# Optimization experiments

Hardware: AMD Instinct MI355X
Metric: run time of the kernel (lower is better)

The kernel has to match this reference:

```python
import jax, jax.numpy as jnp
import numpy as np

N_HEADS = 8
D_EMBED = 64
B, S = 2, 2048
ROPE_BASE = 10000.0


def apply_rope(x):
    # x: [b, h, s, d]; interleaved-pair rotary embedding over the s axis
    d = x.shape[-1]
    s = x.shape[-2]
    inv_freq = 1.0 / (ROPE_BASE ** (jnp.arange(0, d, 2, dtype=jnp.float32) / d))  # [d/2]
    angles = jnp.arange(s, dtype=jnp.float32)[:, None] * inv_freq[None, :]  # [s, d/2]
    cos = jnp.cos(angles)[None, None, :, :]
    sin = jnp.sin(angles)[None, None, :, :]
    x1 = x[..., 0::2]
    x2 = x[..., 1::2]
    out = jnp.stack([x1 * cos - x2 * sin, x1 * sin + x2 * cos], axis=-1)
    return out.reshape(x.shape)


def setup_inputs() -> dict:
    key = jax.random.key(0)
    ks = jax.random.split(key, 7)
    scale = 1.0 / np.sqrt(D_EMBED)
    return {
        "q": jax.random.normal(ks[0], (B, S, D_EMBED), dtype=jnp.float32),
        "k": jax.random.normal(ks[1], (B, S, D_EMBED), dtype=jnp.float32),
        "v": jax.random.normal(ks[2], (B, S, D_EMBED), dtype=jnp.float32),
        "W_q": jax.random.normal(ks[3], (N_HEADS, D_EMBED, D_EMBED), dtype=jnp.float32) * scale,
        "W_k": jax.random.normal(ks[4], (N_HEADS, D_EMBED, D_EMBED), dtype=jnp.float32) * scale,
        "W_v": jax.random.normal(ks[5], (N_HEADS, D_EMBED, D_EMBED), dtype=jnp.float32) * scale,
        "W_o": jax.random.normal(ks[6], (N_HEADS * D_EMBED, D_EMBED), dtype=jnp.float32) * scale,
    }


def reference(q, k, v, W_q, W_k, W_v, W_o):
    Bn, Sn, E = q.shape
    H = W_q.shape[0]
    qh = jnp.einsum('bsz,hzd->bhsd', q, W_q)
    kh = jnp.einsum('bsz,hzd->bhsd', k, W_k)
    vh = jnp.einsum('bsz,hzd->bhsd', v, W_v)
    qh = apply_rope(qh)
    kh = apply_rope(kh)
    attn_scaling = 1.0 / E  # note: 1/d, not 1/sqrt(d), per original
    scores = jnp.einsum('bhqd,bhkd->bhqk', qh, kh)
    causal = jnp.triu(jnp.ones((Sn, Sn), dtype=bool), k=1)
    scores = jnp.where(causal[None, None], -jnp.inf, scores) * attn_scaling
    probs = jax.nn.softmax(scores, axis=-1)
    # post-softmax diagonal zeroing (breaks normalization; this is the ICL twist)
    diag_mask = 1.0 - jnp.eye(Sn, dtype=probs.dtype)
    probs = probs * diag_mask[None, None]
    # NOTE: einsum 'bhzs,bhzd->bhsd' in the original contracts over the QUERY axis
    # (probs transposed): out[k-pos] = sum_q P[q, k-pos] * v[q]
    out = jnp.einsum('bhqk,bhqd->bhkd', probs, vh)
    out = out.transpose(0, 2, 1, 3).reshape(Bn, Sn, H * E)
    return jnp.einsum('bsz,zd->bsd', out, W_o)
```

## Files before the change

kernel.cpp:

```cpp
#include <hip/hip_runtime.h>
#include <hip/hip_bf16.h>
#include <math.h>

#define NH 8
#define D 64
#define BB 2
#define SS 2048
#define NBH (BB*NH)
#define LOG2E 1.4426950408889634f
#define KPAR 8
#define QPAR 4

typedef short bf16x8 __attribute__((ext_vector_type(8)));
typedef float f32x4 __attribute__((ext_vector_type(4)));

#define MFMA16(a,b,c) __builtin_amdgcn_mfma_f32_16x16x32_bf16((a),(b),(c),0,0,0)

__device__ inline int xcd_swz(int orig, int nwg) {
    int cpx = nwg >> 3;
    return (orig & 7) * cpx + (orig >> 3);
}

__device__ inline short f2bf(float f) {
    unsigned u = __float_as_uint(f);
    unsigned r = (u + 0x7fffu + ((u >> 16) & 1u)) >> 16;
    return (short)r;
}
__device__ inline float bf2f(short s) {
    return __uint_as_float(((unsigned)(unsigned short)s) << 16);
}
__device__ inline unsigned pack2bf(float a, float b) {
    __hip_bfloat162 hv = __float22bfloat162_rn(make_float2(a, b));
    unsigned u;
    __builtin_memcpy(&u, &hv, 4);
    return u;
}

__global__ __launch_bounds__(256) void wtrans_kernel(
    const float* __restrict__ Wq, const float* __restrict__ Wk,
    const float* __restrict__ Wv, const float* __restrict__ Wo,
    short* __restrict__ WqT, short* __restrict__ WkT, short* __restrict__ WvT,
    short* __restrict__ WoT) {
    int blk = blockIdx.x;
    int t = threadIdx.x;
    if (blk < 24) {
        int tensor = blk >> 3, h = blk & 7;
        const float* W = tensor == 0 ? Wq : (tensor == 1 ? Wk : Wv);
        short* WT = tensor == 0 ? WqT : (tensor == 1 ? WkT : WvT);
        __shared__ float wl[64][65];
        {
            int z = t >> 2, c0 = (t & 3) * 16;
            const float* src = W + (size_t)h * 4096 + (size_t)z * 64 + c0;
#pragma unroll
            for (int i = 0; i < 16; ++i) wl[z][c0 + i] = src[i];
        }
        __syncthreads();
        {
            int d = t >> 2, z0 = (t & 3) * 16;
            short* dst = WT + ((size_t)h * 64 + d) * 64 + z0;
#pragma unroll
            for (int i = 0; i < 16; ++i) dst[i] = f2bf(wl[z0 + i][d]);
        }
    } else {
        int idx = (blk - 24) * 256 + t;
        int d = idx >> 6;
        int zc = (idx & 63) * 32;
#pragma unroll
        for (int j = 0; j < 32; ++j) {
            int z = zc + j;
            WoT[(size_t)d * 2048 + z] = f2bf(Wo[(size_t)(z & 511) * 64 + d]);
        }
    }
}

__global__ __launch_bounds__(256) void proj_mfma_kernel(
    const float* __restrict__ xq, const float* __restrict__ xk,
    const float* __restrict__ xv,
    const short* __restrict__ WqT, const short* __restrict__ WkT,
    const short* __restrict__ WvT,
    short* __restrict__ qh, short* __restrict__ kh, short* __restrict__ vhT) {
    int blk = xcd_swz(blockIdx.x, 3 * NBH * 32);
    int tensor = blk / (NBH * 32);
    int rem = blk - tensor * (NBH * 32);
    int st = rem & 31, bh = rem >> 5;
    int h = bh & 7, b = bh >> 3;
    const float* x = tensor == 0 ? xq : (tensor == 1 ? xk : xv);
    const short* WT = tensor == 0 ? WqT : (tensor == 1 ? WkT : WvT);

    int t = threadIdx.x, w = t >> 6, lane = t & 63;
    int l15 = lane & 15, lg = lane >> 4;

    __shared__ short vt[64 * 64];

    int sA = st * 64 + w * 16 + l15;
    const float* xr = x + ((size_t)b * SS + sA) * D + lg * 8;
    bf16x8 a0, a1;
#pragma unroll
    for (int j = 0; j < 8; ++j) a0[j] = f2bf(xr[j]);
#pragma unroll
    for (int j = 0; j < 8; ++j) a1[j] = f2bf(xr[32 + j]);

    bf16x8 bfr[4][2];
#pragma unroll
    for (int ds_ = 0; ds_ < 4; ++ds_) {
        int d = ds_ * 16 + l15;
        const short* wp = WT + ((size_t)h * 64 + d) * 64 + lg * 8;
        bfr[ds_][0] = *(const bf16x8*)(wp);
        bfr[ds_][1] = *(const bf16x8*)(wp + 32);
    }

    f32x4 c[4];
#pragma unroll
    for (int ds_ = 0; ds_ < 4; ++ds_) {
        f32x4 z = {0.f, 0.f, 0.f, 0.f};
        z = MFMA16(a0, bfr[ds_][0], z);
        z = MFMA16(a1, bfr[ds_][1], z);
        c[ds_] = z;
    }

    int sbase = st * 64 + w * 16 + lg * 4;
    if (tensor < 2) {
        short* dst = tensor == 0 ? qh : kh;
        float scale = tensor == 0 ? (LOG2E / 64.0f) : 1.0f;
#pragma unroll
        for (int ds_ = 0; ds_ < 4; ++ds_) {
            int d = ds_ * 16 + l15;
            float invf = exp2f(-(float)(d & ~1) * (13.287712379549449f / 64.0f));
#pragma unroll
            for (int r = 0; r < 4; ++r) {
                float v = c[ds_][r];
                float pr = __shfl_xor(v, 1);
                float ang = (float)(sbase + r) * invf;
                float cs = __cosf(ang), sn = __sinf(ang);
                float o = (d & 1) ? (pr * sn + v * cs) : (v * cs - pr * sn);
                dst[((size_t)bh * SS + sbase + r) * D + d] = f2bf(o * scale);
            }
        }
    } else {
#pragma unroll
        for (int ds_ = 0; ds_ < 4; ++ds_) {
            int d = ds_ * 16 + l15;
#pragma unroll
            for (int r = 0; r < 4; ++r) {
                int sc = w * 16 + lg * 4 + r;
                vt[d * 64 + (sc ^ ((d & 7) << 3))] = f2bf(c[ds_][r]);
            }
        }
        __syncthreads();
#pragma unroll
        for (int pp = 0; pp < 2; ++pp) {
            int idx = pp * 256 + t;
            int d = idx >> 3, a = idx & 7;
            bf16x8 val = *(const bf16x8*)&vt[d * 64 + ((a ^ (d & 7)) << 3)];
            *(bf16x8*)&vhT[((size_t)bh * D + d) * SS + st * 64 + a * 8] = val;
        }
    }
}

__global__ __launch_bounds__(256, 4) void colstats_kernel(
    const short* __restrict__ qh, const short* __restrict__ kh,
    float* __restrict__ lpart) {
    int blk = xcd_swz(blockIdx.x, NBH * 64);
    int ph2 = blk & 1, qt = (blk >> 1) & 31, bh = blk >> 6;
    int t = threadIdx.x, w = t >> 6, lane = t & 63;
    int l15 = lane & 15, lg = lane >> 4;
    int pp = ph2 * 4 + w;

    bf16x8 qb[4][2];
#pragma unroll
    for (int qs = 0; qs < 4; ++qs) {
        const short* qp = qh + ((size_t)bh * SS + qt * 64 + qs * 16 + l15) * D + lg * 8;
        qb[qs][0] = *(const bf16x8*)qp;
        qb[qs][1] = *(const bf16x8*)(qp + 32);
    }

    const short* kbase = kh + (size_t)bh * SS * D;
    float lsum[4] = {0.f, 0.f, 0.f, 0.f};

    for (int kt = pp; kt <= qt; kt += KPAR) {
        bool diag = (kt == qt);
#pragma unroll
        for (int ks = 0; ks < 4; ++ks) {
            const short* kp = kbase + (size_t)(kt * 64 + ks * 16 + l15) * D + lg * 8;
            bf16x8 ka0 = *(const bf16x8*)kp;
            bf16x8 ka1 = *(const bf16x8*)(kp + 32);
            int kb = kt * 64 + ks * 16 + lg * 4;
#pragma unroll
            for (int qs = 0; qs < 4; ++qs) {
                f32x4 s = {0.f, 0.f, 0.f, 0.f};
                s = MFMA16(ka0, qb[qs][0], s);
                s = MFMA16(ka1, qb[qs][1], s);
                int qc = qt * 64 + qs * 16 + l15;
#pragma unroll
                for (int r = 0; r < 4; ++r) {
                    float e = (!diag || kb + r <= qc) ? exp2f(s[r]) : 0.f;
                    lsum[qs] += e;
                }
            }
        }
    }
#pragma unroll
    for (int qs = 0; qs < 4; ++qs) {
        lsum[qs] += __shfl_xor(lsum[qs], 16);
        lsum[qs] += __shfl_xor(lsum[qs], 32);
    }
    if (lane < 16) {
#pragma unroll
        for (int qs = 0; qs < 4; ++qs)
            lpart[((size_t)pp * NBH + bh) * SS + qt * 64 + qs * 16 + lane] = lsum[qs];
    }
}

__global__ __launch_bounds__(256) void merge_scale_kernel(
    const float* __restrict__ lpart, short* __restrict__ vhT) {
    int blk = blockIdx.x;
    int qc = blk & 15, bh = blk >> 4;
    int t = threadIdx.x;
    const size_t STR = (size_t)NBH * SS;
    __shared__ float il[128];
    if (t < 128) {
        size_t idx = (size_t)bh * SS + qc * 128 + t;
        float l = 0.f;
#pragma unroll
        for (int pp = 0; pp < KPAR; ++pp) l += lpart[pp * STR + idx];
        il[t] = 1.0f / l;
    }
    __syncthreads();
    int d = t >> 2, sub = t & 3;
    size_t base = ((size_t)bh * 64 + d) * SS + qc * 128 + sub * 32;
#pragma unroll
    for (int j = 0; j < 32; j += 8) {
        bf16x8 v = *(bf16x8*)&vhT[base + j];
#pragma unroll
        for (int jj = 0; jj < 8; ++jj)
            v[jj] = f2bf(bf2f(v[jj]) * il[sub * 32 + j + jj]);
        *(bf16x8*)&vhT[base + j] = v;
    }
}

__global__ __launch_bounds__(256, 4) void pv_kernel(
    const short* __restrict__ qh, const short* __restrict__ kh,
    const short* __restrict__ vhT,
    short* __restrict__ attc) {
    int blk = xcd_swz(blockIdx.x, NBH * 64);
    int ph = blk & 3, p = (blk >> 2) & 15, bh = blk >> 6;
    int h = bh & 7, b = bh >> 3;
    int t = threadIdx.x, w = t >> 6, lane = t & 63;
    int l15 = lane & 15, lg = lane >> 4;
    int kt = (w & 1) ? (31 - p) : p;
    int hf = w >> 1;
    int row0 = kt * 64 + hf * 32;

    __shared__ short pl[4][32 * 64];
    short* plw = pl[w];

    bf16x8 kb[2][2];
#pragma unroll
    for (int kg = 0; kg < 2; ++kg) {
        const short* kp = kh + ((size_t)bh * SS + row0 + kg * 16 + l15) * D + lg * 8;
        kb[kg][0] = *(const bf16x8*)kp;
        kb[kg][1] = *(const bf16x8*)(kp + 32);
    }

    f32x4 acc[2][4];
#pragma unroll
    for (int rg = 0; rg < 2; ++rg)
#pragma unroll
        for (int i = 0; i < 4; ++i) acc[rg][i] = (f32x4){0.f, 0.f, 0.f, 0.f};

    const short* qbase = qh + (size_t)bh * SS * D;
    const short* vbase = vhT + (size_t)bh * D * SS;

    int qt0 = kt + ((ph - kt) & (QPAR - 1));
    for (int qt = qt0; qt < 32; qt += QPAR) {
        bool diag = (qt == kt);
        bf16x8 qa[4][2];
#pragma unroll
        for (int qg = 0; qg < 4; ++qg) {
            const short* qp2 = qbase + (size_t)(qt * 64 + qg * 16 + l15) * D + lg * 8;
            qa[qg][0] = *(const bf16x8*)qp2;
            qa[qg][1] = *(const bf16x8*)(qp2 + 32);
        }
#pragma unroll
        for (int qg = 0; qg < 4; ++qg) {
#pragma unroll
            for (int kg = 0; kg < 2; ++kg) {
                f32x4 s = {0.f, 0.f, 0.f, 0.f};
                s = MFMA16(qa[qg][0], kb[kg][0], s);
                s = MFMA16(qa[qg][1], kb[kg][1], s);
                float p0 = exp2f(s[0]);
                float p1 = exp2f(s[1]);
                float p2 = exp2f(s[2]);
                float p3 = exp2f(s[3]);
                if (diag) {
                    int qoff = qg * 16 + 4 * lg;
                    int kk = hf * 32 + kg * 16 + l15;
                    if (qoff + 0 <= kk) p0 = 0.f;
                    if (qoff + 1 <= kk) p1 = 0.f;
                    if (qoff + 2 <= kk) p2 = 0.f;
                    if (qoff + 3 <= kk) p3 = 0.f;
                }
                unsigned u0 = pack2bf(p0, p1);
                unsigned u1 = pack2bf(p2, p3);
                int row = kg * 16 + l15;
                int col = (qg * 16 + 4 * lg) ^ ((row & 7) << 3);
                uint2 val;
                val.x = u0;
                val.y = u1;
                *(uint2*)&plw[row * 64 + col] = val;
            }
        }
#pragma unroll
        for (int qhh = 0; qhh < 2; ++qhh) {
            int chunk = (qhh << 2) | lg;
            int cc = (chunk ^ (l15 & 7)) << 3;
            bf16x8 pa0 = *(const bf16x8*)&plw[l15 * 64 + cc];
            bf16x8 pa1 = *(const bf16x8*)&plw[(16 + l15) * 64 + cc];
#pragma unroll
            for (int ds_ = 0; ds_ < 4; ++ds_) {
                const short* vp2 = vbase + (size_t)(ds_ * 16 + l15) * SS + qt * 64 + chunk * 8;
                bf16x8 vb = *(const bf16x8*)vp2;
                acc[0][ds_] = MFMA16(pa0, vb, acc[0][ds_]);
                acc[1][ds_] = MFMA16(pa1, vb, acc[1][ds_]);
            }
        }
    }
#pragma unroll
    for (int rg = 0; rg < 2; ++rg)
#pragma unroll
        for (int ds_ = 0; ds_ < 4; ++ds_) {
            int d = ds_ * 16 + l15;
#pragma unroll
            for (int r = 0; r < 4; ++r) {
                int k = row0 + rg * 16 + lg * 4 + r;
                attc[((size_t)b * SS + k) * 2048 + ph * 512 + h * 64 + d] =
                    f2bf(acc[rg][ds_][r]);
            }
        }
}

__global__ __launch_bounds__(256) void outproj_kernel(
    const short* __restrict__ attc, const short* __restrict__ WoT,
    float* __restrict__ out) {
    int blk = blockIdx.x;
    int t = threadIdx.x, w = t >> 6, lane = t & 63;
    int l15 = lane & 15, lg = lane >> 4;
    int srow = blk * 16 + l15;
    const short* arow = attc + (size_t)srow * 2048 + lg * 8;

    f32x4 acc[4];
#pragma unroll
    for (int i = 0; i < 4; ++i) acc[i] = (f32x4){0.f, 0.f, 0.f, 0.f};

#pragma unroll
    for (int i = 0; i < 16; ++i) {
        int kc = w * 16 + i;
        bf16x8 af = *(const bf16x8*)(arow + kc * 32);
#pragma unroll
        for (int ds_ = 0; ds_ < 4; ++ds_) {
            bf16x8 bf_ = *(const bf16x8*)&WoT[(size_t)(ds_ * 16 + l15) * 2048 + kc * 32 + lg * 8];
            acc[ds_] = MFMA16(af, bf_, acc[ds_]);
        }
    }
    __shared__ float red[4][16 * 64];
#pragma unroll
    for (int ds_ = 0; ds_ < 4; ++ds_)
#pragma unroll
        for (int r = 0; r < 4; ++r)
            red[w][(lg * 4 + r) * 64 + ds_ * 16 + l15] = acc[ds_][r];
    __syncthreads();
    {
        int idx4 = t * 4;
        int row = idx4 >> 6, col = idx4 & 63;
        float4 s0 = *(const float4*)&red[0][row * 64 + col];
        float4 s1 = *(const float4*)&red[1][row * 64 + col];
        float4 s2 = *(const float4*)&red[2][row * 64 + col];
        float4 s3 = *(const float4*)&red[3][row * 64 + col];
        float4 sum;
        sum.x = s0.x + s1.x + s2.x + s3.x;
        sum.y = s0.y + s1.y + s2.y + s3.y;
        sum.z = s0.z + s1.z + s2.z + s3.z;
        sum.w = s0.w + s1.w + s2.w + s3.w;
        *(float4*)&out[(size_t)(blk * 16 + row) * 64 + col] = sum;
    }
}

extern "C" void kernel_launch(void* const* d_in, const int* in_sizes, int n_in,
                              void* d_out, int out_size, void* d_ws, size_t ws_size,
                              hipStream_t stream) {
    const float* q  = (const float*)d_in[0];
    const float* k  = (const float*)d_in[1];
    const float* v  = (const float*)d_in[2];
    const float* Wq = (const float*)d_in[3];
    const float* Wk = (const float*)d_in[4];
    const float* Wv = (const float*)d_in[5];
    const float* Wo = (const float*)d_in[6];
    float* out = (float*)d_out;

    const size_t PROJ = (size_t)NBH * SS * D;

    short* qh  = (short*)d_ws;
    short* kh  = qh + PROJ;
    short* vhT = kh + PROJ;
    short* WqT = vhT + PROJ;
    short* WkT = WqT + 32768;
    short* WvT = WkT + 32768;
    short* WoT = WvT + 32768;
    float* lpart = (float*)(WoT + 131072);
    short* attc  = (short*)(lpart + (size_t)KPAR * NBH * SS);

    wtrans_kernel<<<40, 256, 0, stream>>>(Wq, Wk, Wv, Wo, WqT, WkT, WvT, WoT);

    proj_mfma_kernel<<<3 * NBH * 32, 256, 0, stream>>>(q, k, v, WqT, WkT, WvT,
                                                       qh, kh, vhT);

    colstats_kernel<<<NBH * 64, 256, 0, stream>>>(qh, kh, lpart);

    merge_scale_kernel<<<NBH * 16, 256, 0, stream>>>(lpart, vhT);

    pv_kernel<<<NBH * 64, 256, 0, stream>>>(qh, kh, vhT, attc);

    outproj_kernel<<<256, 256, 0, stream>>>(attc, WoT, out);
}
```

Before: 99.54 us.

## Materialize unnormalized probability tiles in colstats and reuse them in pv_kernel

colstats_kernel now writes the masked exp2 score tiles as bf16 into a global triangular buffer (528 tiles per head) while accumulating row sums. pv_kernel reads those tiles instead of recomputing QK^T, exp2 and the mask, and no longer stages them in LDS. This removes the duplicate QK MFMA and exp work. In exchange each head writes and reads about 4 MB of probability data through global memory, and the output depends on the extra workspace being large enough.

```diff
diff --git a/kernel.cpp b/kernel.cpp
--- a/kernel.cpp
+++ b/kernel.cpp
@@ -10,6 +10,7 @@
 #define LOG2E 1.4426950408889634f
 #define KPAR 8
 #define QPAR 4
+#define NTILE 528
 
 typedef short bf16x8 __attribute__((ext_vector_type(8)));
 typedef float f32x4 __attribute__((ext_vector_type(4)));
@@ -34,6 +35,9 @@
     unsigned u;
     __builtin_memcpy(&u, &hv, 4);
     return u;
+}
+__device__ inline int tri_row(int kt) {
+    return kt * 32 - ((kt * (kt - 1)) >> 1) - kt;
 }
 
 __global__ __launch_bounds__(256) void wtrans_kernel(
@@ -159,55 +163,76 @@
 
 __global__ __launch_bounds__(256, 4) void colstats_kernel(
     const short* __restrict__ qh, const short* __restrict__ kh,
-    float* __restrict__ lpart) {
+    float* __restrict__ lpart, short* __restrict__ Pbuf) {
     int blk = xcd_swz(blockIdx.x, NBH * 64);
     int ph2 = blk & 1, qt = (blk >> 1) & 31, bh = blk >> 6;
     int t = threadIdx.x, w = t >> 6, lane = t & 63;
     int l15 = lane & 15, lg = lane >> 4;
     int pp = ph2 * 4 + w;
 
-    bf16x8 qb[4][2];
-#pragma unroll
-    for (int qs = 0; qs < 4; ++qs) {
-        const short* qp = qh + ((size_t)bh * SS + qt * 64 + qs * 16 + l15) * D + lg * 8;
-        qb[qs][0] = *(const bf16x8*)qp;
-        qb[qs][1] = *(const bf16x8*)(qp + 32);
+    bf16x8 qa[4][2];
+#pragma unroll
+    for (int qg = 0; qg < 4; ++qg) {
+        const short* qp = qh + ((size_t)bh * SS + qt * 64 + qg * 16 + l15) * D + lg * 8;
+        qa[qg][0] = *(const bf16x8*)qp;
+        qa[qg][1] = *(const bf16x8*)(qp + 32);
     }
 
     const short* kbase = kh + (size_t)bh * SS * D;
-    float lsum[4] = {0.f, 0.f, 0.f, 0.f};
+    float lsum[4][4];
+#pragma unroll
+    for (int qg = 0; qg < 4; ++qg)
+#pragma unroll
+        for (int r = 0; r < 4; ++r) lsum[qg][r] = 0.f;
 
     for (int kt = pp; kt <= qt; kt += KPAR) {
         bool diag = (kt == qt);
+        size_t tile = ((size_t)bh * NTILE + tri_row(kt) + qt) * 4096;
 #pragma unroll
         for (int ks = 0; ks < 4; ++ks) {
             const short* kp = kbase + (size_t)(kt * 64 + ks * 16 + l15) * D + lg * 8;
-            bf16x8 ka0 = *(const bf16x8*)kp;
-            bf16x8 ka1 = *(const bf16x8*)(kp + 32);
-            int kb = kt * 64 + ks * 16 + lg * 4;
-#pragma unroll
-            for (int qs = 0; qs < 4; ++qs) {
+            bf16x8 kb0 = *(const bf16x8*)kp;
+            bf16x8 kb1 = *(const bf16x8*)(kp + 32);
+            int kv = ks * 16 + l15;
+#pragma unroll
+            for (int qg = 0; qg < 4; ++qg) {
                 f32x4 s = {0.f, 0.f, 0.f, 0.f};
-                s = MFMA16(ka0, qb[qs][0], s);
-                s = MFMA16(ka1, qb[qs][1], s);
-                int qc = qt * 64 + qs * 16 + l15;
+                s = MFMA16(qa[qg][0], kb0, s);
+                s = MFMA16(qa[qg][1], kb1, s);
+                int qv = qg * 16 + 4 * lg;
+                float p0, p1, p2, p3;
 #pragma unroll
                 for (int r = 0; r < 4; ++r) {
-                    float e = (!diag || kb + r <= qc) ? exp2f(s[r]) : 0.f;
-                    lsum[qs] += e;
+                    float ex = exp2f(s[r]);
+                    float e = (diag && kv > qv + r) ? 0.f : ex;
+                    float pv_ = (diag && kv >= qv + r) ? 0.f : ex;
+                    lsum[qg][r] += e;
+                    if (r == 0) p0 = pv_;
+                    else if (r == 1) p1 = pv_;
+                    else if (r == 2) p2 = pv_;
+                    else p3 = pv_;
                 }
+                uint2 val;
+                val.x = pack2bf(p0, p1);
+                val.y = pack2bf(p2, p3);
+                *(uint2*)&Pbuf[tile + (size_t)kv * 64 + qv] = val;
             }
         }
     }
 #pragma unroll
-    for (int qs = 0; qs < 4; ++qs) {
-        lsum[qs] += __shfl_xor(lsum[qs], 16);
-        lsum[qs] += __shfl_xor(lsum[qs], 32);
-    }
-    if (lane < 16) {
-#pragma unroll
-        for (int qs = 0; qs < 4; ++qs)
-            lpart[((size_t)pp * NBH + bh) * SS + qt * 64 + qs * 16 + lane] = lsum[qs];
+    for (int off = 1; off <= 8; off <<= 1)
+#pragma unroll
+        for (int qg = 0; qg < 4; ++qg)
+#pragma unroll
+            for (int r = 0; r < 4; ++r)
+                lsum[qg][r] += __shfl_xor(lsum[qg][r], off);
+    if (l15 == 0) {
+        float* lp = lpart + ((size_t)pp * NBH + bh) * SS + qt * 64 + 4 * lg;
+#pragma unroll
+        for (int qg = 0; qg < 4; ++qg)
+#pragma unroll
+            for (int r = 0; r < 4; ++r)
+                lp[qg * 16 + r] = lsum[qg][r];
     }
 }
 
@@ -239,8 +264,7 @@
 }
 
 __global__ __launch_bounds__(256, 4) void pv_kernel(
-    const short* __restrict__ qh, const short* __restrict__ kh,
-    const short* __restrict__ vhT,
+    const short* __restrict__ Pbuf, const short* __restrict__ vhT,
     short* __restrict__ attc) {
     int blk = xcd_swz(blockIdx.x, NBH * 64);
     int ph = blk & 3, p = (blk >> 2) & 15, bh = blk >> 6;
@@ -251,77 +275,33 @@
     int hf = w >> 1;
     int row0 = kt * 64 + hf * 32;
 
-    __shared__ short pl[4][32 * 64];
-    short* plw = pl[w];
-
-    bf16x8 kb[2][2];
-#pragma unroll
-    for (int kg = 0; kg < 2; ++kg) {
-        const short* kp = kh + ((size_t)bh * SS + row0 + kg * 16 + l15) * D + lg * 8;
-        kb[kg][0] = *(const bf16x8*)kp;
-        kb[kg][1] = *(const bf16x8*)(kp + 32);
-    }
-
     f32x4 acc[2][4];
 #pragma unroll
     for (int rg = 0; rg < 2; ++rg)
 #pragma unroll
         for (int i = 0; i < 4; ++i) acc[rg][i] = (f32x4){0.f, 0.f, 0.f, 0.f};
 
-    const short* qbase = qh + (size_t)bh * SS * D;
     const short* vbase = vhT + (size_t)bh * D * SS;
+    const size_t tb = (size_t)bh * NTILE + tri_row(kt);
+    const size_t arow = (size_t)(hf * 32 + l15) * 64 + lg * 8;
 
     int qt0 = kt + ((ph - kt) & (QPAR - 1));
     for (int qt = qt0; qt < 32; qt += QPAR) {
-        bool diag = (qt == kt);
-        bf16x8 qa[4][2];
-#pragma unroll
-        for (int qg = 0; qg < 4; ++qg) {
-            const short* qp2 = qbase + (size_t)(qt * 64 + qg * 16 + l15) * D + lg * 8;
-            qa[qg][0] = *(const bf16x8*)qp2;
-            qa[qg][1] = *(const bf16x8*)(qp2 + 32);
-        }
-#pragma unroll
-        for (int qg = 0; qg < 4; ++qg) {
-#pragma unroll
-            for (int kg = 0; kg < 2; ++kg) {
-                f32x4 s = {0.f, 0.f, 0.f, 0.f};
-                s = MFMA16(qa[qg][0], kb[kg][0], s);
-                s = MFMA16(qa[qg][1], kb[kg][1], s);
-                float p0 = exp2f(s[0]);
-                float p1 = exp2f(s[1]);
-                float p2 = exp2f(s[2]);
-                float p3 = exp2f(s[3]);
-                if (diag) {
-                    int qoff = qg * 16 + 4 * lg;
-                    int kk = hf * 32 + kg * 16 + l15;
-                    if (qoff + 0 <= kk) p0 = 0.f;
-                    if (qoff + 1 <= kk) p1 = 0.f;
-                    if (qoff + 2 <= kk) p2 = 0.f;
-                    if (qoff + 3 <= kk) p3 = 0.f;
-                }
-                unsigned u0 = pack2bf(p0, p1);
-                unsigned u1 = pack2bf(p2, p3);
-                int row = kg * 16 + l15;
-                int col = (qg * 16 + 4 * lg) ^ ((row & 7) << 3);
-                uint2 val;
-                val.x = u0;
-                val.y = u1;
-                *(uint2*)&plw[row * 64 + col] = val;
-            }
-        }
-#pragma unroll
-        for (int qhh = 0; qhh < 2; ++qhh) {
-            int chunk = (qhh << 2) | lg;
-            int cc = (chunk ^ (l15 & 7)) << 3;
-            bf16x8 pa0 = *(const bf16x8*)&plw[l15 * 64 + cc];
-            bf16x8 pa1 = *(const bf16x8*)&plw[(16 + l15) * 64 + cc];
+        const short* tp = Pbuf + (tb + qt) * 4096 + arow;
+        bf16x8 pa00 = *(const bf16x8*)(tp);
+        bf16x8 pa01 = *(const bf16x8*)(tp + 32);
+        bf16x8 pa10 = *(const bf16x8*)(tp + 1024);
+        bf16x8 pa11 = *(const bf16x8*)(tp + 1024 + 32);
+#pragma unroll
+        for (int half = 0; half < 2; ++half) {
+            bf16x8 a0 = half ? pa01 : pa00;
+            bf16x8 a1 = half ? pa11 : pa10;
 #pragma unroll
             for (int ds_ = 0; ds_ < 4; ++ds_) {
-                const short* vp2 = vbase + (size_t)(ds_ * 16 + l15) * SS + qt * 64 + chunk * 8;
+                const short* vp2 = vbase + (size_t)(ds_ * 16 + l15) * SS + qt * 64 + half * 32 + lg * 8;
                 bf16x8 vb = *(const bf16x8*)vp2;
-                acc[0][ds_] = MFMA16(pa0, vb, acc[0][ds_]);
-                acc[1][ds_] = MFMA16(pa1, vb, acc[1][ds_]);
+                acc[0][ds_] = MFMA16(a0, vb, acc[0][ds_]);
+                acc[1][ds_] = MFMA16(a1, vb, acc[1][ds_]);
             }
         }
     }
@@ -408,17 +388,18 @@
     short* WoT = WvT + 32768;
     float* lpart = (float*)(WoT + 131072);
     short* attc  = (short*)(lpart + (size_t)KPAR * NBH * SS);
+    short* Pbuf  = attc + (size_t)BB * SS * 2048;
 
     wtrans_kernel<<<40, 256, 0, stream>>>(Wq, Wk, Wv, Wo, WqT, WkT, WvT, WoT);
 
     proj_mfma_kernel<<<3 * NBH * 32, 256, 0, stream>>>(q, k, v, WqT, WkT, WvT,
                                                        qh, kh, vhT);
 
-    colstats_kernel<<<NBH * 64, 256, 0, stream>>>(qh, kh, lpart);
+    colstats_kernel<<<NBH * 64, 256, 0, stream>>>(qh, kh, lpart, Pbuf);
 
     merge_scale_kernel<<<NBH * 16, 256, 0, stream>>>(lpart, vhT);
 
-    pv_kernel<<<NBH * 64, 256, 0, stream>>>(qh, kh, vhT, attc);
+    pv_kernel<<<NBH * 64, 256, 0, stream>>>(Pbuf, vhT, attc);
 
     outproj_kernel<<<256, 256, 0, stream>>>(attc, WoT, out);
 }
```

Result: slower. 101.7 us (+2.1%).

## Balance causal work across waves and batch V loads with MFMA priority

Applied to the files above, without the earlier changes.

The column-stats kernel now pairs query tiles qp and 31-qp inside one block, so each block carries a balanced share of the causal triangle, and it batches K-tile loads two at a time. The PV kernel swaps which wave takes the mirrored tile based on the block index. It also hoists all V-fragment loads ahead of the PV MFMAs and raises wave priority with s_setprio around that MFMA section. Together these aim to cut load imbalance from the triangular workload and hide global-load latency, at the cost of more live registers, which could lower occupancy.

```diff
diff --git a/kernel.cpp b/kernel.cpp
--- a/kernel.cpp
+++ b/kernel.cpp
@@ -161,17 +161,19 @@
     const short* __restrict__ qh, const short* __restrict__ kh,
     float* __restrict__ lpart) {
     int blk = xcd_swz(blockIdx.x, NBH * 64);
-    int ph2 = blk & 1, qt = (blk >> 1) & 31, bh = blk >> 6;
+    int ph = blk & 3, qp = (blk >> 2) & 15, bh = blk >> 6;
     int t = threadIdx.x, w = t >> 6, lane = t & 63;
     int l15 = lane & 15, lg = lane >> 4;
-    int pp = ph2 * 4 + w;
+    int qsel = (w ^ (qp >> 3)) & 1;
+    int qt = qsel ? (31 - qp) : qp;
+    int pp = ph * 2 + (w >> 1);
 
     bf16x8 qb[4][2];
 #pragma unroll
     for (int qs = 0; qs < 4; ++qs) {
-        const short* qp = qh + ((size_t)bh * SS + qt * 64 + qs * 16 + l15) * D + lg * 8;
-        qb[qs][0] = *(const bf16x8*)qp;
-        qb[qs][1] = *(const bf16x8*)(qp + 32);
+        const short* qp2 = qh + ((size_t)bh * SS + qt * 64 + qs * 16 + l15) * D + lg * 8;
+        qb[qs][0] = *(const bf16x8*)qp2;
+        qb[qs][1] = *(const bf16x8*)(qp2 + 32);
     }
 
     const short* kbase = kh + (size_t)bh * SS * D;
@@ -180,21 +182,30 @@
     for (int kt = pp; kt <= qt; kt += KPAR) {
         bool diag = (kt == qt);
 #pragma unroll
-        for (int ks = 0; ks < 4; ++ks) {
-            const short* kp = kbase + (size_t)(kt * 64 + ks * 16 + l15) * D + lg * 8;
-            bf16x8 ka0 = *(const bf16x8*)kp;
-            bf16x8 ka1 = *(const bf16x8*)(kp + 32);
-            int kb = kt * 64 + ks * 16 + lg * 4;
-#pragma unroll
-            for (int qs = 0; qs < 4; ++qs) {
-                f32x4 s = {0.f, 0.f, 0.f, 0.f};
-                s = MFMA16(ka0, qb[qs][0], s);
-                s = MFMA16(ka1, qb[qs][1], s);
-                int qc = qt * 64 + qs * 16 + l15;
-#pragma unroll
-                for (int r = 0; r < 4; ++r) {
-                    float e = (!diag || kb + r <= qc) ? exp2f(s[r]) : 0.f;
-                    lsum[qs] += e;
+        for (int ksp = 0; ksp < 2; ++ksp) {
+            bf16x8 ka[2][2];
+#pragma unroll
+            for (int kss = 0; kss < 2; ++kss) {
+                int ks = ksp * 2 + kss;
+                const short* kp = kbase + (size_t)(kt * 64 + ks * 16 + l15) * D + lg * 8;
+                ka[kss][0] = *(const bf16x8*)kp;
+                ka[kss][1] = *(const bf16x8*)(kp + 32);
+            }
+#pragma unroll
+            for (int kss = 0; kss < 2; ++kss) {
+                int ks = ksp * 2 + kss;
+                int kb = kt * 64 + ks * 16 + lg * 4;
+#pragma unroll
+                for (int qs = 0; qs < 4; ++qs) {
+                    f32x4 s = {0.f, 0.f, 0.f, 0.f};
+                    s = MFMA16(ka[kss][0], qb[qs][0], s);
+                    s = MFMA16(ka[kss][1], qb[qs][1], s);
+                    int qc = qt * 64 + qs * 16 + l15;
+#pragma unroll
+                    for (int r = 0; r < 4; ++r) {
+                        float e = (!diag || kb + r <= qc) ? exp2f(s[r]) : 0.f;
+                        lsum[qs] += e;
+                    }
                 }
             }
         }
@@ -247,7 +258,8 @@
     int h = bh & 7, b = bh >> 3;
     int t = threadIdx.x, w = t >> 6, lane = t & 63;
     int l15 = lane & 15, lg = lane >> 4;
-    int kt = (w & 1) ? (31 - p) : p;
+    int sel = (w ^ (p >> 3)) & 1;
+    int kt = sel ? (31 - p) : p;
     int hf = w >> 1;
     int row0 = kt * 64 + hf * 32;
 
@@ -274,42 +286,55 @@
     int qt0 = kt + ((ph - kt) & (QPAR - 1));
     for (int qt = qt0; qt < 32; qt += QPAR) {
         bool diag = (qt == kt);
-        bf16x8 qa[4][2];
-#pragma unroll
-        for (int qg = 0; qg < 4; ++qg) {
-            const short* qp2 = qbase + (size_t)(qt * 64 + qg * 16 + l15) * D + lg * 8;
-            qa[qg][0] = *(const bf16x8*)qp2;
-            qa[qg][1] = *(const bf16x8*)(qp2 + 32);
-        }
-#pragma unroll
-        for (int qg = 0; qg < 4; ++qg) {
-#pragma unroll
-            for (int kg = 0; kg < 2; ++kg) {
-                f32x4 s = {0.f, 0.f, 0.f, 0.f};
-                s = MFMA16(qa[qg][0], kb[kg][0], s);
-                s = MFMA16(qa[qg][1], kb[kg][1], s);
-                float p0 = exp2f(s[0]);
-                float p1 = exp2f(s[1]);
-                float p2 = exp2f(s[2]);
-                float p3 = exp2f(s[3]);
-                if (diag) {
-                    int qoff = qg * 16 + 4 * lg;
-                    int kk = hf * 32 + kg * 16 + l15;
-                    if (qoff + 0 <= kk) p0 = 0.f;
-                    if (qoff + 1 <= kk) p1 = 0.f;
-                    if (qoff + 2 <= kk) p2 = 0.f;
-                    if (qoff + 3 <= kk) p3 = 0.f;
+        {
+            bf16x8 qa[4][2];
+#pragma unroll
+            for (int qg = 0; qg < 4; ++qg) {
+                const short* qp2 = qbase + (size_t)(qt * 64 + qg * 16 + l15) * D + lg * 8;
+                qa[qg][0] = *(const bf16x8*)qp2;
+                qa[qg][1] = *(const bf16x8*)(qp2 + 32);
+            }
+#pragma unroll
+            for (int qg = 0; qg < 4; ++qg) {
+#pragma unroll
+                for (int kg = 0; kg < 2; ++kg) {
+                    f32x4 s = {0.f, 0.f, 0.f, 0.f};
+                    s = MFMA16(qa[qg][0], kb[kg][0], s);
+                    s = MFMA16(qa[qg][1], kb[kg][1], s);
+                    float p0 = exp2f(s[0]);
+                    float p1 = exp2f(s[1]);
+                    float p2 = exp2f(s[2]);
+                    float p3 = exp2f(s[3]);
+                    if (diag) {
+                        int qoff = qg * 16 + 4 * lg;
+                        int kk = hf * 32 + kg * 16 + l15;
+                        if (qoff + 0 <= kk) p0 = 0.f;
+                        if (qoff + 1 <= kk) p1 = 0.f;
+                        if (qoff + 2 <= kk) p2 = 0.f;
+                        if (qoff + 3 <= kk) p3 = 0.f;
+                    }
+                    unsigned u0 = pack2bf(p0, p1);
+                    unsigned u1 = pack2bf(p2, p3);
+                    int row = kg * 16 + l15;
+                    int col = (qg * 16 + 4 * lg) ^ ((row & 7) << 3);
+                    uint2 val;
+                    val.x = u0;
+                    val.y = u1;
+                    *(uint2*)&plw[row * 64 + col] = val;
                 }
-                unsigned u0 = pack2bf(p0, p1);
-                unsigned u1 = pack2bf(p2, p3);
-                int row = kg * 16 + l15;
-                int col = (qg * 16 + 4 * lg) ^ ((row & 7) << 3);
-                uint2 val;
-                val.x = u0;
-                val.y = u1;
-                *(uint2*)&plw[row * 64 + col] = val;
-            }
-        }
+            }
+        }
+        bf16x8 vb[2][4];
+#pragma unroll
+        for (int qhh = 0; qhh < 2; ++qhh) {
+            int chunk = (qhh << 2) | lg;
+#pragma unroll
+            for (int ds_ = 0; ds_ < 4; ++ds_) {
+                const short* vp2 = vbase + (size_t)(ds_ * 16 + l15) * SS + qt * 64 + chunk * 8;
+                vb[qhh][ds_] = *(const bf16x8*)vp2;
+            }
+        }
+        __builtin_amdgcn_s_setprio(1);
 #pragma unroll
         for (int qhh = 0; qhh < 2; ++qhh) {
             int chunk = (qhh << 2) | lg;
@@ -318,13 +343,13 @@
             bf16x8 pa1 = *(const bf16x8*)&plw[(16 + l15) * 64 + cc];
 #pragma unroll
             for (int ds_ = 0; ds_ < 4; ++ds_) {
-                const short* vp2 = vbase + (size_t)(ds_ * 16 + l15) * SS + qt * 64 + chunk * 8;
-                bf16x8 vb = *(const bf16x8*)vp2;
-                acc[0][ds_] = MFMA16(pa0, vb, acc[0][ds_]);
-                acc[1][ds_] = MFMA16(pa1, vb, acc[1][ds_]);
-            }
-        }
-    }
+                acc[0][ds_] = MFMA16(pa0, vb[qhh][ds_], acc[0][ds_]);
+                acc[1][ds_] = MFMA16(pa1, vb[qhh][ds_], acc[1][ds_]);
+            }
+        }
+        __builtin_amdgcn_s_setprio(0);
+    }
+
 #pragma unroll
     for (int rg = 0; rg < 2; ++rg)
 #pragma unroll
```

Measured after the change: 99.20 us. About the same (-0.3%).
